# Performance work log

Measured on AMD Instinct MI355X. Metric: run time of the kernel, lower is better.

The kernel has to match this reference:

```python
import jax, jax.numpy as jnp
import numpy as np

B, D, H, N, M, K = 128, 256, 4, 256, 256, 10  # M=256 is hardcoded in the original repeat(1,1,1,256)
DIM = D // H  # per-head dim = 64


def setup_inputs() -> dict:
    key = jax.random.key(0)
    ks = jax.random.split(key, 10)
    s = 0.05  # weight scale
    return {
        "x": jax.random.normal(ks[0], (B, D, N), jnp.float32),
        "source": jax.random.normal(ks[1], (B, D, M), jnp.float32),
        "Wq": jax.random.normal(ks[2], (D, D), jnp.float32) * s,
        "bq": jax.random.normal(ks[3], (D,), jnp.float32) * s,
        "Wk": jax.random.normal(ks[4], (D, D), jnp.float32) * s,
        "bk": jax.random.normal(ks[5], (D,), jnp.float32) * s,
        "Wv": jax.random.normal(ks[6], (D, D), jnp.float32) * s,
        "bv": jax.random.normal(ks[7], (D,), jnp.float32) * s,
        "Wm": jax.random.normal(ks[8], (D, D), jnp.float32) * s,
        "bm": jax.random.normal(ks[9], (D,), jnp.float32) * s,
        "k": K,
    }


def _pointwise(W, b, x):
    # nn.Conv1d(d, d, kernel_size=1): per-point linear over channel dim
    return jnp.einsum('ef,bfn->ben', W, x) + b[None, :, None]


def reference(x, source, Wq, bq, Wk, bk, Wv, bv, Wm, bm, k):
    b, d, n = x.shape
    # torch .view(b, dim, heads, -1) splits channels as (dim, heads)
    q = _pointwise(Wq, bq, x).reshape(b, DIM, H, n)
    kk = _pointwise(Wk, bk, source).reshape(b, DIM, H, -1)
    v = _pointwise(Wv, bv, source).reshape(b, DIM, H, -1)

    scores = jnp.einsum('bdhn,bdhm->bhnm', q, kk) / jnp.sqrt(jnp.asarray(DIM, x.dtype))
    # per-row top-k threshold: keep only scores >= k-th largest, softmax over kept
    thresh = jax.lax.top_k(scores, k)[0][..., k - 1:k]  # [b,h,n,1]
    mask = scores >= thresh
    neg = jnp.finfo(scores.dtype).min
    prob = jax.nn.softmax(jnp.where(mask, scores, neg), axis=-1)
    prob = jnp.where(mask, prob, jnp.zeros((), scores.dtype))

    out = jnp.einsum('bhnm,bdhm->bdhn', prob, v).reshape(b, d, n)
    return _pointwise(Wm, bm, out)
```

## Files before the change

### kernel.cpp

```cpp
#include <hip/hip_runtime.h>
#include <hip/hip_bf16.h>

#define BB   128
#define DDIM 256
#define HH   4
#define NNN  256
#define MMM  256

typedef __hip_bfloat16 bf16;
typedef short  short8   __attribute__((ext_vector_type(8)));
typedef unsigned short ushort8_t __attribute__((ext_vector_type(8)));
typedef float  f32x4    __attribute__((ext_vector_type(4)));

__device__ __forceinline__ unsigned short f2bf(float x) {
    unsigned u = __builtin_bit_cast(unsigned, x);
    u += 0x7FFFu + ((u >> 16) & 1u);
    return (unsigned short)(u >> 16);
}
__device__ __forceinline__ float bf2f(unsigned short b) {
    unsigned u = ((unsigned)b) << 16;
    return __builtin_bit_cast(float, u);
}

__device__ __forceinline__ void xpose4(float v[4], const int p) {
    float ta = __shfl_xor((p & 1) ? v[0] : v[1], 1, 64);
    float tb = __shfl_xor((p & 1) ? v[2] : v[3], 1, 64);
    float u0 = (p & 1) ? ta : v[0];
    float u1 = (p & 1) ? v[1] : ta;
    float u2 = (p & 1) ? tb : v[2];
    float u3 = (p & 1) ? v[3] : tb;
    float tc = __shfl_xor((p & 2) ? u0 : u2, 2, 64);
    float td = __shfl_xor((p & 2) ? u1 : u3, 2, 64);
    v[0] = (p & 2) ? tc : u0;
    v[1] = (p & 2) ? td : u1;
    v[2] = (p & 2) ? u2 : tc;
    v[3] = (p & 2) ? u3 : td;
}

__device__ __forceinline__ void split3_pack_store(char* dh, char* dm, char* dl,
                                                  const float v[4]) {
    unsigned short h[4], m[4], l[4];
    #pragma unroll
    for (int i = 0; i < 4; ++i) {
        h[i] = f2bf(v[i]);
        float r1 = v[i] - bf2f(h[i]);
        m[i] = f2bf(r1);
        float r2 = r1 - bf2f(m[i]);
        l[i] = f2bf(r2);
    }
    uint2 hp, mp, lp;
    hp.x = (unsigned)h[0] | ((unsigned)h[1] << 16);
    hp.y = (unsigned)h[2] | ((unsigned)h[3] << 16);
    mp.x = (unsigned)m[0] | ((unsigned)m[1] << 16);
    mp.y = (unsigned)m[2] | ((unsigned)m[3] << 16);
    lp.x = (unsigned)l[0] | ((unsigned)l[1] << 16);
    lp.y = (unsigned)l[2] | ((unsigned)l[3] << 16);
    *(uint2*)dh = hp;
    *(uint2*)dm = mp;
    *(uint2*)dl = lp;
}

__device__ __forceinline__ void split2_store(char* dst, const float v[4]) {
    unsigned short h[4], m[4];
    #pragma unroll
    for (int i = 0; i < 4; ++i) {
        h[i] = f2bf(v[i]);
        float r1 = v[i] - bf2f(h[i]);
        m[i] = f2bf(r1);
    }
    uint2 hp, mp;
    hp.x = (unsigned)h[0] | ((unsigned)h[1] << 16);
    hp.y = (unsigned)h[2] | ((unsigned)h[3] << 16);
    mp.x = (unsigned)m[0] | ((unsigned)m[1] << 16);
    mp.y = (unsigned)m[2] | ((unsigned)m[3] << 16);
    *(uint2*)dst = hp;
    *(uint2*)(dst + 16384) = mp;
}

__device__ __forceinline__ void ldx4(const float* p, float v[4]) {
    const float4 f = *(const float4*)p;
    v[0] = f.x; v[1] = f.y; v[2] = f.z; v[3] = f.w;
}
__device__ __forceinline__ void ldx4(const bf16* p, float v[4]) {
    uint2 u = *(const uint2*)p;
    v[0] = bf2f((unsigned short)(u.x & 0xFFFF));
    v[1] = bf2f((unsigned short)(u.x >> 16));
    v[2] = bf2f((unsigned short)(u.y & 0xFFFF));
    v[3] = bf2f((unsigned short)(u.y >> 16));
}

__device__ __forceinline__ float max16v(const float* w) {
    float a = fmaxf(fmaxf(w[0], w[1]),  fmaxf(w[2], w[3]));
    float b = fmaxf(fmaxf(w[4], w[5]),  fmaxf(w[6], w[7]));
    float c = fmaxf(fmaxf(w[8], w[9]),  fmaxf(w[10], w[11]));
    float d = fmaxf(fmaxf(w[12], w[13]), fmaxf(w[14], w[15]));
    return fmaxf(fmaxf(a, b), fmaxf(c, d));
}
__device__ __forceinline__ float gmax16(float v) {
    v = fmaxf(v, __shfl_xor(v, 1, 64));
    v = fmaxf(v, __shfl_xor(v, 2, 64));
    v = fmaxf(v, __shfl_xor(v, 4, 64));
    v = fmaxf(v, __shfl_xor(v, 8, 64));
    return v;
}
__device__ __forceinline__ float gsum16(float v) {
    v += __shfl_xor(v, 1, 64);
    v += __shfl_xor(v, 2, 64);
    v += __shfl_xor(v, 4, 64);
    v += __shfl_xor(v, 8, 64);
    return v;
}

template <typename TIN, typename TOUT>
__global__ __launch_bounds__(512, 2)
void projm_kernel(const TIN* __restrict__ X, const float* __restrict__ W,
                  const float* __restrict__ bias, TOUT* __restrict__ Y) {
    extern __shared__ __align__(16) char smem[];

    const int t    = threadIdx.x;
    const int lane = t & 63;
    const int w    = t >> 6;
    const int c16  = lane & 15;
    const int g    = (lane >> 4) & 3;
    const int p    = lane & 3;
    const int G    = lane >> 2;

    const int n0 = blockIdx.x * 128;
    const int e0 = blockIdx.y * 128;
    const int b  = blockIdx.z;
    const size_t plane = (size_t)b * DDIM * NNN;

    f32x4 acc[8];
    #pragma unroll
    for (int nf = 0; nf < 8; ++nf) acc[nf] = f32x4{0.f, 0.f, 0.f, 0.f};

    #pragma unroll
    for (int ft = 0; ft < 4; ++ft) {
        const int f0 = ft * 64;
        if (ft) __syncthreads();
        #pragma unroll
        for (int it = 0; it < 4; ++it) {
            int chunk = w + 8 * it;
            int fch = chunk & 15, nh = chunk >> 4;
            float v[4];
            ldx4(&X[plane + (size_t)(f0 + fch * 4 + p) * NNN + n0 + nh * 64 + G * 4], v);
            xpose4(v, p);
            int nl = nh * 64 + G * 4 + p;
            int base = nl * 128 + ((fch * 8) ^ ((nl & 7) << 4));
            split2_store(smem + base, v);
        }
        #pragma unroll
        for (int it = 0; it < 4; ++it) {
            int idx = t + 512 * it;
            int el = idx >> 4, fq = idx & 15;
            float v[4];
            const float4 f4 = *(const float4*)&W[(size_t)(e0 + el) * DDIM + f0 + fq * 4];
            v[0] = f4.x; v[1] = f4.y; v[2] = f4.z; v[3] = f4.w;
            int base = 32768 + el * 128 + ((fq * 8) ^ ((el & 7) << 4));
            split2_store(smem + base, v);
        }
        __syncthreads();

        const int ew = w * 16;
        short8 a0[2], a1[2];
        #pragma unroll
        for (int ks = 0; ks < 2; ++ks) {
            int off = 32768 + (ew + c16) * 128
                    + ((ks * 64 + g * 16) ^ ((c16 & 7) << 4));
            a0[ks] = *(const short8*)(smem + off);
            a1[ks] = *(const short8*)(smem + off + 16384);
        }
        #pragma unroll
        for (int nf = 0; nf < 8; ++nf) {
            #pragma unroll
            for (int ks = 0; ks < 2; ++ks) {
                int off = (nf * 16 + c16) * 128
                        + ((ks * 64 + g * 16) ^ ((c16 & 7) << 4));
                short8 b0 = *(const short8*)(smem + off);
                short8 b1 = *(const short8*)(smem + off + 16384);
                f32x4 a = acc[nf];
                a = __builtin_amdgcn_mfma_f32_16x16x32_bf16(a0[ks], b0, a, 0, 0, 0);
                a = __builtin_amdgcn_mfma_f32_16x16x32_bf16(a0[ks], b1, a, 0, 0, 0);
                a = __builtin_amdgcn_mfma_f32_16x16x32_bf16(a1[ks], b0, a, 0, 0, 0);
                acc[nf] = a;
            }
        }
    }

    const int ew = w * 16;
    float bs[4];
    #pragma unroll
    for (int r = 0; r < 4; ++r) bs[r] = bias[e0 + ew + g * 4 + r];
    #pragma unroll
    for (int nf = 0; nf < 8; ++nf) {
        #pragma unroll
        for (int r = 0; r < 4; ++r) {
            size_t off = plane + (size_t)(e0 + ew + g * 4 + r) * NNN + n0 + nf * 16 + c16;
            float val = acc[nf][r] + bs[r];
            if constexpr (sizeof(TOUT) == 4) Y[off] = val;
            else                             *(unsigned short*)&Y[off] = f2bf(val);
        }
    }
}

template <typename TIN, typename TOUT>
__global__ __launch_bounds__(256)
void proj_kernel(const TIN* __restrict__ X, const float* __restrict__ W,
                 const float* __restrict__ bias, TOUT* __restrict__ Y) {
    __shared__ float Wt[32][68];
    __shared__ float Xt[32][68];

    const int t  = threadIdx.x;
    const int tx = t & 15;
    const int ty = t >> 4;
    const int n0 = blockIdx.x * 64;
    const int e0 = blockIdx.y * 64;
    const int b  = blockIdx.z;
    const size_t plane = (size_t)b * DDIM * NNN;

    float acc[4][4] = {};

    for (int f0 = 0; f0 < DDIM; f0 += 32) {
        #pragma unroll
        for (int i = 0; i < 8; ++i) {
            int idx = t + i * 256;
            int fl = idx & 31, el = idx >> 5;
            Wt[fl][el] = W[(size_t)(e0 + el) * DDIM + f0 + fl];
        }
        #pragma unroll
        for (int i = 0; i < 8; ++i) {
            int idx = t + i * 256;
            int nl = idx & 63, fl = idx >> 6;
            Xt[fl][nl] = X[plane + (size_t)(f0 + fl) * NNN + n0 + nl];
        }
        __syncthreads();

        #pragma unroll
        for (int ff = 0; ff < 32; ++ff) {
            const float4 av = *(const float4*)&Wt[ff][ty * 4];
            const float4 bv = *(const float4*)&Xt[ff][tx * 4];
            const float a[4] = {av.x, av.y, av.z, av.w};
            const float c[4] = {bv.x, bv.y, bv.z, bv.w};
            #pragma unroll
            for (int i2 = 0; i2 < 4; ++i2)
                #pragma unroll
                for (int j = 0; j < 4; ++j)
                    acc[i2][j] = fmaf(a[i2], c[j], acc[i2][j]);
        }
        __syncthreads();
    }

    #pragma unroll
    for (int i2 = 0; i2 < 4; ++i2) {
        const int e = e0 + ty * 4 + i2;
        const float bs = bias[e];
        const size_t off = plane + (size_t)e * NNN + n0 + tx * 4;
        float4 o;
        o.x = acc[i2][0] + bs; o.y = acc[i2][1] + bs;
        o.z = acc[i2][2] + bs; o.w = acc[i2][3] + bs;
        *(float4*)&Y[off] = o;
    }
}

template <int NF>
__device__ __forceinline__ void softmax_half(f32x4 (&acc)[2][16], const float (&thr)[2][4],
                                             const float (&rmx)[2][4], char* smem,
                                             int w, int lane, int g, int c16) {
    #pragma unroll
    for (int mf = 0; mf < 16; ++mf) {
        #pragma unroll
        for (int r = 0; r < 4; ++r) {
            float a = acc[NF][mf][r];
            acc[NF][mf][r] = (a >= thr[NF][r]) ? __expf(a - rmx[NF][r]) : 0.f;
        }
    }
    float inv_[4];
    #pragma unroll
    for (int r = 0; r < 4; ++r) {
        float s = ((acc[NF][0][r] + acc[NF][1][r]) + (acc[NF][2][r] + acc[NF][3][r]))
                + ((acc[NF][4][r] + acc[NF][5][r]) + (acc[NF][6][r] + acc[NF][7][r]))
                + ((acc[NF][8][r] + acc[NF][9][r]) + (acc[NF][10][r] + acc[NF][11][r]))
                + ((acc[NF][12][r] + acc[NF][13][r]) + (acc[NF][14][r] + acc[NF][15][r]));
        s = gsum16(s);
        inv_[r] = 1.0f / s;
    }
    #pragma unroll
    for (int mf = 0; mf < 16; ++mf) {
        #pragma unroll
        for (int r = 0; r < 4; ++r) {
            int row = w * 16 + g * 4 + r;
            int m2  = (mf * 16 + c16) * 2;
            int off = row * 512 + (m2 ^ ((row & 7) << 4));
            *(unsigned short*)(smem + off) = f2bf(acc[NF][mf][r] * inv_[r]);
        }
    }
}

template <int NF>
__device__ __forceinline__ void pv_half(f32x4 (&o)[2][4], const char* smem,
                                        int w, int lane, int c16) {
    short8 pa[8];
    #pragma unroll
    for (int ks = 0; ks < 8; ++ks) {
        int row = w * 16 + c16;
        int off = row * 512 + ((ks * 64 + (lane >> 4) * 16) ^ ((row & 7) << 4));
        pa[ks] = *(const short8*)(smem + off);
    }
    #pragma unroll
    for (int df = 0; df < 4; ++df) {
        f32x4 o_ = {0.f, 0.f, 0.f, 0.f};
        #pragma unroll
        for (int ks = 0; ks < 8; ++ks) {
            int d = df * 16 + c16;
            int off = 32768 + d * 512 + ((ks * 64 + (lane >> 4) * 16) ^ ((d & 7) << 4));
            short8 vv = *(const short8*)(smem + off);
            o_ = __builtin_amdgcn_mfma_f32_16x16x32_bf16(pa[ks], vv, o_, 0, 0, 0);
        }
        o[NF][df] = o_;
    }
}

__global__ __launch_bounds__(256, 2)
void attn2_kernel(const float* __restrict__ qf, const float* __restrict__ kf,
                  const bf16* __restrict__ vb, bf16* __restrict__ ob,
                  const int* __restrict__ kptr) {
    extern __shared__ __align__(16) char smem[];

    const int t    = threadIdx.x;
    const int lane = t & 63;
    const int w    = t >> 6;
    const int g    = lane >> 4;
    const int c16  = lane & 15;

    const int i    = blockIdx.x;
    const int work = (i & 7) * 128 + (i >> 3);
    const int bx = work & 1;
    const int h  = (work >> 1) & 3;
    const int b  = work >> 3;
    const int n0 = bx * 128;

    const size_t planeF = (size_t)b * DDIM * NNN;
    const size_t planeV = (size_t)b * DDIM * MMM;

    int kk = kptr[0];
    kk = kk < 1 ? 1 : (kk > MMM ? MMM : kk);

    {
        const int p = lane & 3, G = lane >> 2;
        #pragma unroll
        for (int it = 0; it < 8; ++it) {
            int chunk = w + 4 * it;
            int dch = chunk & 15, nh = chunk >> 4;
            int drow = dch * 4 + p;
            int ncol = n0 + nh * 64 + G * 4;
            float v[4];
            const float4 f4 = *(const float4*)&qf[planeF + (size_t)(drow * HH + h) * NNN + ncol];
            v[0] = f4.x * 0.125f; v[1] = f4.y * 0.125f;
            v[2] = f4.z * 0.125f; v[3] = f4.w * 0.125f;
            xpose4(v, p);
            int nl = nh * 64 + G * 4 + p;
            int base = nl * 128 + ((dch * 8) ^ ((nl & 7) << 4));
            split3_pack_store(smem + base, smem + 16384 + base, smem + 32768 + base, v);
        }
    }
    __syncthreads();

    short8 qh[2][2], qm[2][2], ql[2][2];
    #pragma unroll
    for (int nf = 0; nf < 2; ++nf) {
        #pragma unroll
        for (int ks = 0; ks < 2; ++ks) {
            int nl = w * 32 + nf * 16 + c16;
            int off = nl * 128 + ((ks * 64 + (lane >> 4) * 16) ^ ((nl & 7) << 4));
            qh[nf][ks] = *(const short8*)(smem + off);
            qm[nf][ks] = *(const short8*)(smem + 16384 + off);
            ql[nf][ks] = *(const short8*)(smem + 32768 + off);
        }
    }

    f32x4 acc[2][16];
    #pragma unroll
    for (int a = 0; a < 2; ++a)
        #pragma unroll
        for (int m = 0; m < 16; ++m)
            acc[a][m] = f32x4{0.f, 0.f, 0.f, 0.f};

    #pragma unroll
    for (int tt = 0; tt < 4; ++tt) {
        {
            const int p = lane & 3, G = lane >> 2;
            #pragma unroll
            for (int it = 0; it < 4; ++it) {
                int chunk = w + 4 * it;
                int drow = chunk * 4 + p;
                int mcol = tt * 64 + G * 4;
                float v[4];
                const float4 f4 = *(const float4*)&kf[planeF + (size_t)(drow * HH + h) * MMM + mcol];
                v[0] = f4.x; v[1] = f4.y; v[2] = f4.z; v[3] = f4.w;
                xpose4(v, p);
                int ml = G * 4 + p;
                int base = ml * 128 + ((chunk * 8) ^ ((ml & 7) << 4));
                split3_pack_store(smem + 49152 + base, smem + 57344 + base,
                                  smem + 65536 + base, v);
            }
        }
        __syncthreads();
        #pragma unroll
        for (int mf = 0; mf < 4; ++mf) {
            #pragma unroll
            for (int ks = 0; ks < 2; ++ks) {
                int ml = mf * 16 + c16;
                int off = ml * 128 + ((ks * 64 + (lane >> 4) * 16) ^ ((ml & 7) << 4));
                short8 bh = *(const short8*)(smem + 49152 + off);
                short8 bm = *(const short8*)(smem + 57344 + off);
                short8 bl = *(const short8*)(smem + 65536 + off);
                #pragma unroll
                for (int nf = 0; nf < 2; ++nf) {
                    f32x4 a = acc[nf][tt * 4 + mf];
                    a = __builtin_amdgcn_mfma_f32_16x16x32_bf16(qh[nf][ks], bh, a, 0, 0, 0);
                    a = __builtin_amdgcn_mfma_f32_16x16x32_bf16(qh[nf][ks], bm, a, 0, 0, 0);
                    a = __builtin_amdgcn_mfma_f32_16x16x32_bf16(qm[nf][ks], bh, a, 0, 0, 0);
                    a = __builtin_amdgcn_mfma_f32_16x16x32_bf16(qm[nf][ks], bm, a, 0, 0, 0);
                    a = __builtin_amdgcn_mfma_f32_16x16x32_bf16(qh[nf][ks], bl, a, 0, 0, 0);
                    a = __builtin_amdgcn_mfma_f32_16x16x32_bf16(ql[nf][ks], bh, a, 0, 0, 0);
                    acc[nf][tt * 4 + mf] = a;
                }
            }
        }
        __syncthreads();
    }

    ushort8_t vreg[8];
    #pragma unroll
    for (int it = 0; it < 8; ++it) {
        int idx = t + it * 256;
        int d = idx >> 5, mc = idx & 31;
        vreg[it] = *(const ushort8_t*)&vb[planeV + (size_t)(d * HH + h) * MMM + mc * 8];
    }

    float thr[2][4], rmx[2][4];
    #pragma unroll
    for (int nf = 0; nf < 2; ++nf) {
        #pragma unroll
        for (int r = 0; r < 4; ++r) {
            float w16[16];
            #pragma unroll
            for (int mf = 0; mf < 16; ++mf) w16[mf] = acc[nf][mf][r];
            float lm = max16v(w16);
            float gm = gmax16(lm);
            rmx[nf][r] = gm;
            for (int it = 1; it < kk; ++it) {
                unsigned long long bal = __ballot(lm == gm);
                unsigned gmask = (unsigned)((bal >> (g * 16)) & 0xFFFFull);
                int leader = __builtin_ctz(gmask);
                bool skip = (c16 != leader);
                #pragma unroll
                for (int mf = 0; mf < 16; ++mf) {
                    bool hit = (!skip) && (w16[mf] == gm);
                    w16[mf] = hit ? -INFINITY : w16[mf];
                    skip = skip || hit;
                }
                lm = max16v(w16);
                gm = gmax16(lm);
            }
            thr[nf][r] = gm;
        }
    }

    softmax_half<0>(acc, thr, rmx, smem, w, lane, g, c16);
    #pragma unroll
    for (int it = 0; it < 8; ++it) {
        int idx = t + it * 256;
        int d = idx >> 5, mc = idx & 31;
        int off = 32768 + d * 512 + ((mc * 16) ^ ((d & 7) << 4));
        *(ushort8_t*)(smem + off) = vreg[it];
    }
    __syncthreads();

    f32x4 o[2][4];
    pv_half<0>(o, smem, w, lane, c16);
    __syncthreads();
    softmax_half<1>(acc, thr, rmx, smem, w, lane, g, c16);
    __syncthreads();
    pv_half<1>(o, smem, w, lane, c16);
    __syncthreads();

    #pragma unroll
    for (int nf = 0; nf < 2; ++nf)
        #pragma unroll
        for (int df = 0; df < 4; ++df)
            #pragma unroll
            for (int r = 0; r < 4; ++r) {
                int d  = df * 16 + c16;
                int nl = w * 32 + nf * 16 + g * 4 + r;
                int off = d * 256 + ((nl * 2) ^ ((d & 7) << 4));
                *(unsigned short*)(smem + off) = f2bf(o[nf][df][r]);
            }
    __syncthreads();
    #pragma unroll
    for (int it = 0; it < 4; ++it) {
        int idx = t + it * 256;
        int d = idx >> 4, ch = idx & 15;
        int off = d * 256 + ((ch * 16) ^ ((d & 7) << 4));
        ushort8_t val = *(const ushort8_t*)(smem + off);
        *(ushort8_t*)&ob[planeV + (size_t)(d * HH + h) * NNN + n0 + ch * 8] = val;
    }
}

extern "C" void kernel_launch(void* const* d_in, const int* in_sizes, int n_in,
                              void* d_out, int out_size, void* d_ws, size_t ws_size,
                              hipStream_t stream) {
    const float* x   = (const float*)d_in[0];
    const float* src = (const float*)d_in[1];
    const float* Wq  = (const float*)d_in[2];
    const float* bq  = (const float*)d_in[3];
    const float* Wk  = (const float*)d_in[4];
    const float* bk  = (const float*)d_in[5];
    const float* Wv  = (const float*)d_in[6];
    const float* bv  = (const float*)d_in[7];
    const float* Wm  = (const float*)d_in[8];
    const float* bm  = (const float*)d_in[9];
    const int*   kp  = (const int*)d_in[10];
    float* out = (float*)d_out;

    const size_t F32PLANE  = (size_t)BB * DDIM * NNN * sizeof(float);
    const size_t BF16PLANE = F32PLANE / 2;
    char* ws = (char*)d_ws;
    float* qf = (float*)(ws);
    float* kf = (float*)(ws + F32PLANE);
    bf16*  vb = (bf16*)(ws + 2 * F32PLANE);
    bf16*  ob = (bf16*)(ws + 2 * F32PLANE + BF16PLANE);

    hipFuncSetAttribute((const void*)(projm_kernel<float, bf16>),
                        hipFuncAttributeMaxDynamicSharedMemorySize, 65536);
    hipFuncSetAttribute((const void*)(projm_kernel<bf16, float>),
                        hipFuncAttributeMaxDynamicSharedMemorySize, 65536);
    hipFuncSetAttribute((const void*)attn2_kernel,
                        hipFuncAttributeMaxDynamicSharedMemorySize, 73728);

    dim3 fgrid(NNN / 64, DDIM / 64, BB);
    hipLaunchKernelGGL((proj_kernel<float, float>), fgrid, dim3(256), 0, stream,
                       x,   Wq, bq, qf);
    hipLaunchKernelGGL((proj_kernel<float, float>), fgrid, dim3(256), 0, stream,
                       src, Wk, bk, kf);

    dim3 mgrid(2, 2, BB);
    hipLaunchKernelGGL((projm_kernel<float, bf16>), mgrid, dim3(512), 65536, stream,
                       src, Wv, bv, vb);

    hipLaunchKernelGGL(attn2_kernel, dim3(1024), dim3(256), 73728, stream,
                       qf, kf, vb, ob, kp);

    hipLaunchKernelGGL((projm_kernel<bf16, float>), mgrid, dim3(512), 65536, stream,
                       ob, Wm, bm, out);
}
```

Before: 290.0 us.

## Split attention blocks to 64 query rows, stream V in halves, widen fp32 projection tiles

The attention kernel now handles 64 query rows per block instead of 128, launching 2048 blocks with 48KB of shared memory and a launch bound of 3 blocks per CU, where it was 72KB before. Register use per thread also drops because each wave keeps one set of accumulators instead of two. V is loaded through shared memory in two 128-column halves rather than prefetched into registers. The fp32 Q/K projection kernel now computes 64x128 tiles with float4 loads, for more reuse per thread. The trade-off is that each K tile is loaded and split twice as many times in total, and there are more barriers.

```diff
diff --git a/kernel.cpp b/kernel.cpp
--- a/kernel.cpp
+++ b/kernel.cpp
@@ -37,8 +37,7 @@
     v[3] = (p & 2) ? u3 : td;
 }
 
-__device__ __forceinline__ void split3_pack_store(char* dh, char* dm, char* dl,
-                                                  const float v[4]) {
+__device__ __forceinline__ void split3_store8k(char* dst, const float v[4]) {
     unsigned short h[4], m[4], l[4];
     #pragma unroll
     for (int i = 0; i < 4; ++i) {
@@ -55,9 +54,9 @@
     mp.y = (unsigned)m[2] | ((unsigned)m[3] << 16);
     lp.x = (unsigned)l[0] | ((unsigned)l[1] << 16);
     lp.y = (unsigned)l[2] | ((unsigned)l[3] << 16);
-    *(uint2*)dh = hp;
-    *(uint2*)dm = mp;
-    *(uint2*)dl = lp;
+    *(uint2*)dst = hp;
+    *(uint2*)(dst + 8192) = mp;
+    *(uint2*)(dst + 16384) = lp;
 }
 
 __device__ __forceinline__ void split2_store(char* dst, const float v[4]) {
@@ -109,6 +108,66 @@
     v += __shfl_xor(v, 4, 64);
     v += __shfl_xor(v, 8, 64);
     return v;
+}
+
+__global__ __launch_bounds__(256)
+void proj_kernel(const float* __restrict__ X, const float* __restrict__ W,
+                 const float* __restrict__ bias, float* __restrict__ Y) {
+    __shared__ float Wt[32][68];
+    __shared__ float Xt[32][132];
+
+    const int t  = threadIdx.x;
+    const int tx = t & 31;
+    const int ty = t >> 5;
+    const int n0 = blockIdx.x * 128;
+    const int e0 = blockIdx.y * 64;
+    const int b  = blockIdx.z;
+    const size_t plane = (size_t)b * DDIM * NNN;
+
+    float acc[8][4] = {};
+
+    for (int f0 = 0; f0 < DDIM; f0 += 32) {
+        #pragma unroll
+        for (int i = 0; i < 8; ++i) {
+            int idx = t + i * 256;
+            int fl = idx & 31, el = idx >> 5;
+            Wt[fl][el] = W[(size_t)(e0 + el) * DDIM + f0 + fl];
+        }
+        #pragma unroll
+        for (int i = 0; i < 4; ++i) {
+            int idx = t + i * 256;
+            int fl = idx >> 5, nl4 = idx & 31;
+            *(float4*)&Xt[fl][nl4 * 4] =
+                *(const float4*)&X[plane + (size_t)(f0 + fl) * NNN + n0 + nl4 * 4];
+        }
+        __syncthreads();
+
+        #pragma unroll
+        for (int ff = 0; ff < 32; ++ff) {
+            const float4 av0 = *(const float4*)&Wt[ff][ty * 8];
+            const float4 av1 = *(const float4*)&Wt[ff][ty * 8 + 4];
+            const float4 bv  = *(const float4*)&Xt[ff][tx * 4];
+            const float a[8] = {av0.x, av0.y, av0.z, av0.w, av1.x, av1.y, av1.z, av1.w};
+            const float c[4] = {bv.x, bv.y, bv.z, bv.w};
+            #pragma unroll
+            for (int i2 = 0; i2 < 8; ++i2)
+                #pragma unroll
+                for (int j = 0; j < 4; ++j)
+                    acc[i2][j] = fmaf(a[i2], c[j], acc[i2][j]);
+        }
+        __syncthreads();
+    }
+
+    #pragma unroll
+    for (int i2 = 0; i2 < 8; ++i2) {
+        const int e = e0 + ty * 8 + i2;
+        const float bs = bias[e];
+        const size_t off = plane + (size_t)e * NNN + n0 + tx * 4;
+        float4 o;
+        o.x = acc[i2][0] + bs; o.y = acc[i2][1] + bs;
+        o.z = acc[i2][2] + bs; o.w = acc[i2][3] + bs;
+        *(float4*)&Y[off] = o;
+    }
 }
 
 template <typename TIN, typename TOUT>
@@ -203,125 +262,8 @@
     }
 }
 
-template <typename TIN, typename TOUT>
-__global__ __launch_bounds__(256)
-void proj_kernel(const TIN* __restrict__ X, const float* __restrict__ W,
-                 const float* __restrict__ bias, TOUT* __restrict__ Y) {
-    __shared__ float Wt[32][68];
-    __shared__ float Xt[32][68];
-
-    const int t  = threadIdx.x;
-    const int tx = t & 15;
-    const int ty = t >> 4;
-    const int n0 = blockIdx.x * 64;
-    const int e0 = blockIdx.y * 64;
-    const int b  = blockIdx.z;
-    const size_t plane = (size_t)b * DDIM * NNN;
-
-    float acc[4][4] = {};
-
-    for (int f0 = 0; f0 < DDIM; f0 += 32) {
-        #pragma unroll
-        for (int i = 0; i < 8; ++i) {
-            int idx = t + i * 256;
-            int fl = idx & 31, el = idx >> 5;
-            Wt[fl][el] = W[(size_t)(e0 + el) * DDIM + f0 + fl];
-        }
-        #pragma unroll
-        for (int i = 0; i < 8; ++i) {
-            int idx = t + i * 256;
-            int nl = idx & 63, fl = idx >> 6;
-            Xt[fl][nl] = X[plane + (size_t)(f0 + fl) * NNN + n0 + nl];
-        }
-        __syncthreads();
-
-        #pragma unroll
-        for (int ff = 0; ff < 32; ++ff) {
-            const float4 av = *(const float4*)&Wt[ff][ty * 4];
-            const float4 bv = *(const float4*)&Xt[ff][tx * 4];
-            const float a[4] = {av.x, av.y, av.z, av.w};
-            const float c[4] = {bv.x, bv.y, bv.z, bv.w};
-            #pragma unroll
-            for (int i2 = 0; i2 < 4; ++i2)
-                #pragma unroll
-                for (int j = 0; j < 4; ++j)
-                    acc[i2][j] = fmaf(a[i2], c[j], acc[i2][j]);
-        }
-        __syncthreads();
-    }
-
-    #pragma unroll
-    for (int i2 = 0; i2 < 4; ++i2) {
-        const int e = e0 + ty * 4 + i2;
-        const float bs = bias[e];
-        const size_t off = plane + (size_t)e * NNN + n0 + tx * 4;
-        float4 o;
-        o.x = acc[i2][0] + bs; o.y = acc[i2][1] + bs;
-        o.z = acc[i2][2] + bs; o.w = acc[i2][3] + bs;
-        *(float4*)&Y[off] = o;
-    }
-}
-
-template <int NF>
-__device__ __forceinline__ void softmax_half(f32x4 (&acc)[2][16], const float (&thr)[2][4],
-                                             const float (&rmx)[2][4], char* smem,
-                                             int w, int lane, int g, int c16) {
-    #pragma unroll
-    for (int mf = 0; mf < 16; ++mf) {
-        #pragma unroll
-        for (int r = 0; r < 4; ++r) {
-            float a = acc[NF][mf][r];
-            acc[NF][mf][r] = (a >= thr[NF][r]) ? __expf(a - rmx[NF][r]) : 0.f;
-        }
-    }
-    float inv_[4];
-    #pragma unroll
-    for (int r = 0; r < 4; ++r) {
-        float s = ((acc[NF][0][r] + acc[NF][1][r]) + (acc[NF][2][r] + acc[NF][3][r]))
-                + ((acc[NF][4][r] + acc[NF][5][r]) + (acc[NF][6][r] + acc[NF][7][r]))
-                + ((acc[NF][8][r] + acc[NF][9][r]) + (acc[NF][10][r] + acc[NF][11][r]))
-                + ((acc[NF][12][r] + acc[NF][13][r]) + (acc[NF][14][r] + acc[NF][15][r]));
-        s = gsum16(s);
-        inv_[r] = 1.0f / s;
-    }
-    #pragma unroll
-    for (int mf = 0; mf < 16; ++mf) {
-        #pragma unroll
-        for (int r = 0; r < 4; ++r) {
-            int row = w * 16 + g * 4 + r;
-            int m2  = (mf * 16 + c16) * 2;
-            int off = row * 512 + (m2 ^ ((row & 7) << 4));
-            *(unsigned short*)(smem + off) = f2bf(acc[NF][mf][r] * inv_[r]);
-        }
-    }
-}
-
-template <int NF>
-__device__ __forceinline__ void pv_half(f32x4 (&o)[2][4], const char* smem,
-                                        int w, int lane, int c16) {
-    short8 pa[8];
-    #pragma unroll
-    for (int ks = 0; ks < 8; ++ks) {
-        int row = w * 16 + c16;
-        int off = row * 512 + ((ks * 64 + (lane >> 4) * 16) ^ ((row & 7) << 4));
-        pa[ks] = *(const short8*)(smem + off);
-    }
-    #pragma unroll
-    for (int df = 0; df < 4; ++df) {
-        f32x4 o_ = {0.f, 0.f, 0.f, 0.f};
-        #pragma unroll
-        for (int ks = 0; ks < 8; ++ks) {
-            int d = df * 16 + c16;
-            int off = 32768 + d * 512 + ((ks * 64 + (lane >> 4) * 16) ^ ((d & 7) << 4));
-            short8 vv = *(const short8*)(smem + off);
-            o_ = __builtin_amdgcn_mfma_f32_16x16x32_bf16(pa[ks], vv, o_, 0, 0, 0);
-        }
-        o[NF][df] = o_;
-    }
-}
-
-__global__ __launch_bounds__(256, 2)
-void attn2_kernel(const float* __restrict__ qf, const float* __restrict__ kf,
+__global__ __launch_bounds__(256, 3)
+void attn3_kernel(const float* __restrict__ qf, const float* __restrict__ kf,
                   const bf16* __restrict__ vb, bf16* __restrict__ ob,
                   const int* __restrict__ kptr) {
     extern __shared__ __align__(16) char smem[];
@@ -333,11 +275,11 @@
     const int c16  = lane & 15;
 
     const int i    = blockIdx.x;
-    const int work = (i & 7) * 128 + (i >> 3);
-    const int bx = work & 1;
-    const int h  = (work >> 1) & 3;
-    const int b  = work >> 3;
-    const int n0 = bx * 128;
+    const int work = (i & 7) * 256 + (i >> 3);
+    const int bx = work & 3;
+    const int h  = (work >> 2) & 3;
+    const int b  = work >> 4;
+    const int n0 = bx * 64;
 
     const size_t planeF = (size_t)b * DDIM * NNN;
     const size_t planeV = (size_t)b * DDIM * MMM;
@@ -348,60 +290,52 @@
     {
         const int p = lane & 3, G = lane >> 2;
         #pragma unroll
-        for (int it = 0; it < 8; ++it) {
-            int chunk = w + 4 * it;
-            int dch = chunk & 15, nh = chunk >> 4;
+        for (int it = 0; it < 4; ++it) {
+            int dch = w + 4 * it;
             int drow = dch * 4 + p;
-            int ncol = n0 + nh * 64 + G * 4;
             float v[4];
-            const float4 f4 = *(const float4*)&qf[planeF + (size_t)(drow * HH + h) * NNN + ncol];
+            const float4 f4 = *(const float4*)&qf[planeF + (size_t)(drow * HH + h) * NNN + n0 + G * 4];
             v[0] = f4.x * 0.125f; v[1] = f4.y * 0.125f;
             v[2] = f4.z * 0.125f; v[3] = f4.w * 0.125f;
             xpose4(v, p);
-            int nl = nh * 64 + G * 4 + p;
+            int nl = G * 4 + p;
             int base = nl * 128 + ((dch * 8) ^ ((nl & 7) << 4));
-            split3_pack_store(smem + base, smem + 16384 + base, smem + 32768 + base, v);
+            split3_store8k(smem + base, v);
         }
     }
     __syncthreads();
 
-    short8 qh[2][2], qm[2][2], ql[2][2];
-    #pragma unroll
-    for (int nf = 0; nf < 2; ++nf) {
-        #pragma unroll
-        for (int ks = 0; ks < 2; ++ks) {
-            int nl = w * 32 + nf * 16 + c16;
-            int off = nl * 128 + ((ks * 64 + (lane >> 4) * 16) ^ ((nl & 7) << 4));
-            qh[nf][ks] = *(const short8*)(smem + off);
-            qm[nf][ks] = *(const short8*)(smem + 16384 + off);
-            ql[nf][ks] = *(const short8*)(smem + 32768 + off);
-        }
-    }
-
-    f32x4 acc[2][16];
-    #pragma unroll
-    for (int a = 0; a < 2; ++a)
-        #pragma unroll
-        for (int m = 0; m < 16; ++m)
-            acc[a][m] = f32x4{0.f, 0.f, 0.f, 0.f};
+    short8 qh[2], qm[2], ql[2];
+    #pragma unroll
+    for (int ks = 0; ks < 2; ++ks) {
+        int nl = w * 16 + c16;
+        int off = nl * 128 + ((ks * 64 + g * 16) ^ ((nl & 7) << 4));
+        qh[ks] = *(const short8*)(smem + off);
+        qm[ks] = *(const short8*)(smem + 8192 + off);
+        ql[ks] = *(const short8*)(smem + 16384 + off);
+    }
+
+    f32x4 acc[16];
+    #pragma unroll
+    for (int m = 0; m < 16; ++m) acc[m] = f32x4{0.f, 0.f, 0.f, 0.f};
 
     #pragma unroll
     for (int tt = 0; tt < 4; ++tt) {
+        if (tt) __syncthreads();
         {
             const int p = lane & 3, G = lane >> 2;
             #pragma unroll
             for (int it = 0; it < 4; ++it) {
-                int chunk = w + 4 * it;
-                int drow = chunk * 4 + p;
+                int dch = w + 4 * it;
+                int drow = dch * 4 + p;
                 int mcol = tt * 64 + G * 4;
                 float v[4];
                 const float4 f4 = *(const float4*)&kf[planeF + (size_t)(drow * HH + h) * MMM + mcol];
                 v[0] = f4.x; v[1] = f4.y; v[2] = f4.z; v[3] = f4.w;
                 xpose4(v, p);
                 int ml = G * 4 + p;
-                int base = ml * 128 + ((chunk * 8) ^ ((ml & 7) << 4));
-                split3_pack_store(smem + 49152 + base, smem + 57344 + base,
-                                  smem + 65536 + base, v);
+                int base = 24576 + ml * 128 + ((dch * 8) ^ ((ml & 7) << 4));
+                split3_store8k(smem + base, v);
             }
         }
         __syncthreads();
@@ -410,98 +344,133 @@
             #pragma unroll
             for (int ks = 0; ks < 2; ++ks) {
                 int ml = mf * 16 + c16;
-                int off = ml * 128 + ((ks * 64 + (lane >> 4) * 16) ^ ((ml & 7) << 4));
-                short8 bh = *(const short8*)(smem + 49152 + off);
-                short8 bm = *(const short8*)(smem + 57344 + off);
-                short8 bl = *(const short8*)(smem + 65536 + off);
-                #pragma unroll
-                for (int nf = 0; nf < 2; ++nf) {
-                    f32x4 a = acc[nf][tt * 4 + mf];
-                    a = __builtin_amdgcn_mfma_f32_16x16x32_bf16(qh[nf][ks], bh, a, 0, 0, 0);
-                    a = __builtin_amdgcn_mfma_f32_16x16x32_bf16(qh[nf][ks], bm, a, 0, 0, 0);
-                    a = __builtin_amdgcn_mfma_f32_16x16x32_bf16(qm[nf][ks], bh, a, 0, 0, 0);
-                    a = __builtin_amdgcn_mfma_f32_16x16x32_bf16(qm[nf][ks], bm, a, 0, 0, 0);
-                    a = __builtin_amdgcn_mfma_f32_16x16x32_bf16(qh[nf][ks], bl, a, 0, 0, 0);
-                    a = __builtin_amdgcn_mfma_f32_16x16x32_bf16(ql[nf][ks], bh, a, 0, 0, 0);
-                    acc[nf][tt * 4 + mf] = a;
-                }
+                int off = 24576 + ml * 128 + ((ks * 64 + g * 16) ^ ((ml & 7) << 4));
+                short8 bh = *(const short8*)(smem + off);
+                short8 bm = *(const short8*)(smem + 8192 + off);
+                short8 bl = *(const short8*)(smem + 16384 + off);
+                f32x4 a = acc[tt * 4 + mf];
+                a = __builtin_amdgcn_mfma_f32_16x16x32_bf16(qh[ks], bh, a, 0, 0, 0);
+                a = __builtin_amdgcn_mfma_f32_16x16x32_bf16(qh[ks], bm, a, 0, 0, 0);
+                a = __builtin_amdgcn_mfma_f32_16x16x32_bf16(qm[ks], bh, a, 0, 0, 0);
+                a = __builtin_amdgcn_mfma_f32_16x16x32_bf16(qm[ks], bm, a, 0, 0, 0);
+                a = __builtin_amdgcn_mfma_f32_16x16x32_bf16(qh[ks], bl, a, 0, 0, 0);
+                a = __builtin_amdgcn_mfma_f32_16x16x32_bf16(ql[ks], bh, a, 0, 0, 0);
+                acc[tt * 4 + mf] = a;
             }
         }
+    }
+    __syncthreads();
+
+    float thr[4], rmx[4];
+    #pragma unroll
+    for (int r = 0; r < 4; ++r) {
+        float w16[16];
+        #pragma unroll
+        for (int mf = 0; mf < 16; ++mf) w16[mf] = acc[mf][r];
+        float lm = max16v(w16);
+        float gm = gmax16(lm);
+        rmx[r] = gm;
+        for (int it = 1; it < kk; ++it) {
+            unsigned long long bal = __ballot(lm == gm);
+            unsigned gmask = (unsigned)((bal >> (g * 16)) & 0xFFFFull);
+            int leader = __builtin_ctz(gmask);
+            bool skip = (c16 != leader);
+            #pragma unroll
+            for (int mf = 0; mf < 16; ++mf) {
+                bool hit = (!skip) && (w16[mf] == gm);
+                w16[mf] = hit ? -INFINITY : w16[mf];
+                skip = skip || hit;
+            }
+            lm = max16v(w16);
+            gm = gmax16(lm);
+        }
+        thr[r] = gm;
+    }
+
+    #pragma unroll
+    for (int mf = 0; mf < 16; ++mf) {
+        #pragma unroll
+        for (int r = 0; r < 4; ++r) {
+            float a = acc[mf][r];
+            acc[mf][r] = (a >= thr[r]) ? __expf(a - rmx[r]) : 0.f;
+        }
+    }
+    float inv_[4];
+    #pragma unroll
+    for (int r = 0; r < 4; ++r) {
+        float s = ((acc[0][r] + acc[1][r]) + (acc[2][r] + acc[3][r]))
+                + ((acc[4][r] + acc[5][r]) + (acc[6][r] + acc[7][r]))
+                + ((acc[8][r] + acc[9][r]) + (acc[10][r] + acc[11][r]))
+                + ((acc[12][r] + acc[13][r]) + (acc[14][r] + acc[15][r]));
+        s = gsum16(s);
+        inv_[r] = 1.0f / s;
+    }
+    #pragma unroll
+    for (int mf = 0; mf < 16; ++mf) {
+        #pragma unroll
+        for (int r = 0; r < 4; ++r) {
+            int row = w * 16 + g * 4 + r;
+            int m2  = (mf * 16 + c16) * 2;
+            int off = row * 512 + (m2 ^ ((row & 7) << 4));
+            *(unsigned short*)(smem + off) = f2bf(acc[mf][r] * inv_[r]);
+        }
+    }
+
+    f32x4 o[4];
+    #pragma unroll
+    for (int df = 0; df < 4; ++df) o[df] = f32x4{0.f, 0.f, 0.f, 0.f};
+
+    #pragma unroll
+    for (int half = 0; half < 2; ++half) {
+        if (half) __syncthreads();
+        #pragma unroll
+        for (int it = 0; it < 4; ++it) {
+            int idx = t + it * 256;
+            int d = idx >> 4, mc8 = idx & 15;
+            ushort8_t val = *(const ushort8_t*)
+                &vb[planeV + (size_t)(d * HH + h) * MMM + half * 128 + mc8 * 8];
+            int off = 32768 + d * 256 + ((mc8 * 16) ^ ((d & 7) << 4));
+            *(ushort8_t*)(smem + off) = val;
+        }
         __syncthreads();
-    }
-
-    ushort8_t vreg[8];
-    #pragma unroll
-    for (int it = 0; it < 8; ++it) {
+
+        short8 pa[4];
+        #pragma unroll
+        for (int ks = 0; ks < 4; ++ks) {
+            int row = w * 16 + c16;
+            int off = row * 512 + ((half * 256 + ks * 64 + g * 16) ^ ((row & 7) << 4));
+            pa[ks] = *(const short8*)(smem + off);
+        }
+        #pragma unroll
+        for (int df = 0; df < 4; ++df) {
+            int d = df * 16 + c16;
+            f32x4 o_ = o[df];
+            #pragma unroll
+            for (int ks = 0; ks < 4; ++ks) {
+                int off = 32768 + d * 256 + ((ks * 64 + g * 16) ^ ((d & 7) << 4));
+                short8 vv = *(const short8*)(smem + off);
+                o_ = __builtin_amdgcn_mfma_f32_16x16x32_bf16(pa[ks], vv, o_, 0, 0, 0);
+            }
+            o[df] = o_;
+        }
+    }
+    __syncthreads();
+
+    #pragma unroll
+    for (int df = 0; df < 4; ++df)
+        #pragma unroll
+        for (int r = 0; r < 4; ++r) {
+            int d  = df * 16 + c16;
+            int nl = w * 16 + g * 4 + r;
+            int off = d * 128 + ((nl * 2) ^ ((d & 7) << 4));
+            *(unsigned short*)(smem + off) = f2bf(o[df][r]);
+        }
+    __syncthreads();
+    #pragma unroll
+    for (int it = 0; it < 2; ++it) {
         int idx = t + it * 256;
-        int d = idx >> 5, mc = idx & 31;
-        vreg[it] = *(const ushort8_t*)&vb[planeV + (size_t)(d * HH + h) * MMM + mc * 8];
-    }
-
-    float thr[2][4], rmx[2][4];
-    #pragma unroll
-    for (int nf = 0; nf < 2; ++nf) {
-        #pragma unroll
-        for (int r = 0; r < 4; ++r) {
-            float w16[16];
-            #pragma unroll
-            for (int mf = 0; mf < 16; ++mf) w16[mf] = acc[nf][mf][r];
-            float lm = max16v(w16);
-            float gm = gmax16(lm);
-            rmx[nf][r] = gm;
-            for (int it = 1; it < kk; ++it) {
-                unsigned long long bal = __ballot(lm == gm);
-                unsigned gmask = (unsigned)((bal >> (g * 16)) & 0xFFFFull);
-                int leader = __builtin_ctz(gmask);
-                bool skip = (c16 != leader);
-                #pragma unroll
-                for (int mf = 0; mf < 16; ++mf) {
-                    bool hit = (!skip) && (w16[mf] == gm);
-                    w16[mf] = hit ? -INFINITY : w16[mf];
-                    skip = skip || hit;
-                }
-                lm = max16v(w16);
-                gm = gmax16(lm);
-            }
-            thr[nf][r] = gm;
-        }
-    }
-
-    softmax_half<0>(acc, thr, rmx, smem, w, lane, g, c16);
-    #pragma unroll
-    for (int it = 0; it < 8; ++it) {
-        int idx = t + it * 256;
-        int d = idx >> 5, mc = idx & 31;
-        int off = 32768 + d * 512 + ((mc * 16) ^ ((d & 7) << 4));
-        *(ushort8_t*)(smem + off) = vreg[it];
-    }
-    __syncthreads();
-
-    f32x4 o[2][4];
-    pv_half<0>(o, smem, w, lane, c16);
-    __syncthreads();
-    softmax_half<1>(acc, thr, rmx, smem, w, lane, g, c16);
-    __syncthreads();
-    pv_half<1>(o, smem, w, lane, c16);
-    __syncthreads();
-
-    #pragma unroll
-    for (int nf = 0; nf < 2; ++nf)
-        #pragma unroll
-        for (int df = 0; df < 4; ++df)
-            #pragma unroll
-            for (int r = 0; r < 4; ++r) {
-                int d  = df * 16 + c16;
-                int nl = w * 32 + nf * 16 + g * 4 + r;
-                int off = d * 256 + ((nl * 2) ^ ((d & 7) << 4));
-                *(unsigned short*)(smem + off) = f2bf(o[nf][df][r]);
-            }
-    __syncthreads();
-    #pragma unroll
-    for (int it = 0; it < 4; ++it) {
-        int idx = t + it * 256;
-        int d = idx >> 4, ch = idx & 15;
-        int off = d * 256 + ((ch * 16) ^ ((d & 7) << 4));
+        int d = idx >> 3, ch = idx & 7;
+        int off = d * 128 + ((ch * 16) ^ ((d & 7) << 4));
         ushort8_t val = *(const ushort8_t*)(smem + off);
         *(ushort8_t*)&ob[planeV + (size_t)(d * HH + h) * NNN + n0 + ch * 8] = val;
     }
@@ -535,20 +504,18 @@
                         hipFuncAttributeMaxDynamicSharedMemorySize, 65536);
     hipFuncSetAttribute((const void*)(projm_kernel<bf16, float>),
                         hipFuncAttributeMaxDynamicSharedMemorySize, 65536);
-    hipFuncSetAttribute((const void*)attn2_kernel,
-                        hipFuncAttributeMaxDynamicSharedMemorySize, 73728);
-
-    dim3 fgrid(NNN / 64, DDIM / 64, BB);
-    hipLaunchKernelGGL((proj_kernel<float, float>), fgrid, dim3(256), 0, stream,
-                       x,   Wq, bq, qf);
-    hipLaunchKernelGGL((proj_kernel<float, float>), fgrid, dim3(256), 0, stream,
-                       src, Wk, bk, kf);
+    hipFuncSetAttribute((const void*)attn3_kernel,
+                        hipFuncAttributeMaxDynamicSharedMemorySize, 49152);
+
+    dim3 fgrid(NNN / 128, DDIM / 64, BB);
+    hipLaunchKernelGGL(proj_kernel, fgrid, dim3(256), 0, stream, x,   Wq, bq, qf);
+    hipLaunchKernelGGL(proj_kernel, fgrid, dim3(256), 0, stream, src, Wk, bk, kf);
 
     dim3 mgrid(2, 2, BB);
     hipLaunchKernelGGL((projm_kernel<float, bf16>), mgrid, dim3(512), 65536, stream,
                        src, Wv, bv, vb);
 
-    hipLaunchKernelGGL(attn2_kernel, dim3(1024), dim3(256), 73728, stream,
+    hipLaunchKernelGGL(attn3_kernel, dim3(2048), dim3(256), 49152, stream,
                        qf, kf, vb, ob, kp);
 
     hipLaunchKernelGGL((projm_kernel<bf16, float>), mgrid, dim3(512), 65536, stream,
```

After: 280.4 us. -3.3%, faster.
